# Kernel optimization log

Hardware: AMD Instinct MI355X
Metric: run time of the kernel (lower is better)

Reference implementation:

```python
import jax, jax.numpy as jnp
import numpy as np

DIM = 512
HEADS = 8
DIM_HEAD = 64
HIDDEN = HEADS * DIM_HEAD  # 512
B, N, M = 4, 2048, 2048


def setup_inputs() -> dict:
    key = jax.random.key(0)
    ks = jax.random.split(key, 7)
    s = 0.02
    return {
        "x": jax.random.normal(ks[0], (B, N, DIM), jnp.float32),
        "context": jax.random.normal(ks[1], (B, M, DIM), jnp.float32),
        "Wq": jax.random.normal(ks[2], (DIM, HIDDEN), jnp.float32) * s,
        "Wk": jax.random.normal(ks[3], (DIM, HIDDEN), jnp.float32) * s,
        "Wv": jax.random.normal(ks[4], (DIM, HIDDEN), jnp.float32) * s,
        "Wo": jax.random.normal(ks[5], (HIDDEN, DIM), jnp.float32) * s,
        "bo": jnp.zeros((DIM,), jnp.float32),
    }


def reference(x, context, Wq, Wk, Wv, Wo, bo):
    scale = DIM_HEAD ** (-0.5)
    # projections: [B, N, HIDDEN] -> [B, H, N, D]
    def split_heads(t):
        b, n, _ = t.shape
        return t.reshape(b, n, HEADS, DIM_HEAD).transpose(0, 2, 1, 3)
    q = split_heads(x @ Wq)
    k = split_heads(context @ Wk)
    v = split_heads(context @ Wv)
    # scores: [B, H, N, M]
    sim = jnp.einsum('bhid,bhjd->bhij', q, k) * scale
    attn = jax.nn.softmax(sim, axis=-1)
    out = jnp.einsum('bhij,bhjd->bhid', attn, v)  # [B, H, N, D]
    out = out.transpose(0, 2, 1, 3).reshape(x.shape[0], x.shape[1], HIDDEN)
    return out @ Wo + bo
```

## Files before the change

### kernel.cpp

```cpp
#include <hip/hip_runtime.h>
#include <hip/hip_bf16.h>


typedef __attribute__((ext_vector_type(8))) short bf16x8;
typedef __attribute__((ext_vector_type(4))) float f32x4;

#define MFMA16(a, b, c) __builtin_amdgcn_mfma_f32_16x16x32_bf16(a, b, c, 0, 0, 0)
#define SCALE_LOG2E 0.18033688011112042f

static __device__ inline unsigned short f2b(float f) {
    __hip_bfloat16 h = __float2bfloat16(f);
    return __builtin_bit_cast(unsigned short, h);
}
static __device__ inline unsigned int pk_rnd(float hi, float lo) {
    unsigned uh = __builtin_bit_cast(unsigned, hi) + 0x8000u;
    unsigned ul = __builtin_bit_cast(unsigned, lo) + 0x8000u;
    return __builtin_amdgcn_perm(uh, ul, 0x07060302);
}
static __device__ inline float fexp2(float x) {
    float r;
    asm("v_exp_f32 %0, %1" : "=v"(r) : "v"(x));
    return r;
}
static __device__ inline void gll16(const void* g, void* l) {
    __builtin_amdgcn_global_load_lds(
        (const __attribute__((address_space(1))) void*)g,
        (__attribute__((address_space(3))) void*)l, 16, 0, 0);
}

__global__ __launch_bounds__(256) void prep_kernel(const float* __restrict__ x,
                                                   const float* __restrict__ ctx,
                                                   const float* __restrict__ Wq,
                                                   const float* __restrict__ Wk,
                                                   const float* __restrict__ Wv,
                                                   const float* __restrict__ Wo,
                                                   unsigned short* __restrict__ xb,
                                                   unsigned short* __restrict__ cb,
                                                   unsigned short* __restrict__ wt_base) {
    __shared__ float T[64][65];
    const int bid = blockIdx.x, tid = threadIdx.x;
    if (bid < 8192) {
        const float* src = (bid < 4096) ? x : ctx;
        unsigned short* dst = (bid < 4096) ? xb : cb;
        int i = (bid & 4095) * 256 + tid;
        const float4 v = reinterpret_cast<const float4*>(src)[i];
        uint2 o;
        o.x = pk_rnd(v.y, v.x);
        o.y = pk_rnd(v.w, v.z);
        reinterpret_cast<uint2*>(dst)[i] = o;
        return;
    }
    const int b = bid - 8192;
    const int which = b >> 6, t6 = b & 63;
    const float* W = (which == 0) ? Wq : (which == 1) ? Wk : (which == 2) ? Wv : Wo;
    unsigned short* Wt = wt_base + (size_t)which * 512 * 512;
    const int n0 = (t6 & 7) * 64, k0 = (t6 >> 3) * 64;
    const int rr = tid >> 4, cc = (tid & 15) * 4;
    #pragma unroll
    for (int i = 0; i < 4; i++) {
        const float4 v = *reinterpret_cast<const float4*>(&W[(size_t)(k0 + rr + 16 * i) * 512 + n0 + cc]);
        T[rr + 16 * i][cc + 0] = v.x; T[rr + 16 * i][cc + 1] = v.y;
        T[rr + 16 * i][cc + 2] = v.z; T[rr + 16 * i][cc + 3] = v.w;
    }
    __syncthreads();
    #pragma unroll
    for (int i = 0; i < 4; i++) {
        int n = rr + 16 * i;
        uint2 o;
        o.x = pk_rnd(T[cc + 1][n], T[cc + 0][n]);
        o.y = pk_rnd(T[cc + 3][n], T[cc + 2][n]);
        *reinterpret_cast<uint2*>(&Wt[(size_t)(n0 + n) * 512 + k0 + cc]) = o;
    }
}

__device__ inline void gemm_tile_128(const unsigned short* __restrict__ A,
                                     const unsigned short* __restrict__ Bt,
                                     int row0, int col0, f32x4 acc[4][4]) {
    __shared__ unsigned short As[128 * 32];
    __shared__ unsigned short Bs[128 * 32];
    const int tid  = threadIdx.x;
    const int lane = tid & 63, wave = tid >> 6;
    const int quad = lane >> 4, mr = lane & 15;
    const int m_off = (wave & 1) * 64, n_off = (wave >> 1) * 64;

    const int lrow = lane >> 2;
    const int lq   = (lane & 3) ^ (lrow & 3);
    const unsigned short* aSrc = A  + (size_t)(row0 + wave * 32 + lrow) * 512 + lq * 8;
    const unsigned short* bSrc = Bt + (size_t)(col0 + wave * 32 + lrow) * 512 + lq * 8;
    unsigned short* aL0 = &As[(wave * 32) * 32];
    unsigned short* aL1 = &As[(wave * 32 + 16) * 32];
    unsigned short* bL0 = &Bs[(wave * 32) * 32];
    unsigned short* bL1 = &Bs[(wave * 32 + 16) * 32];

    for (int kt = 0; kt < 16; kt++) {
        __syncthreads();
        gll16(aSrc + kt * 32, aL0);
        gll16(aSrc + 16 * 512 + kt * 32, aL1);
        gll16(bSrc + kt * 32, bL0);
        gll16(bSrc + 16 * 512 + kt * 32, bL1);
        __syncthreads();
        bf16x8 af[4], bfr[4];
        #pragma unroll
        for (int i = 0; i < 4; i++) {
            int m = m_off + i * 16 + mr;
            af[i] = *reinterpret_cast<const bf16x8*>(&As[m * 32 + ((quad ^ (m & 3)) * 8)]);
        }
        #pragma unroll
        for (int j = 0; j < 4; j++) {
            int n = n_off + j * 16 + mr;
            bfr[j] = *reinterpret_cast<const bf16x8*>(&Bs[n * 32 + ((quad ^ (n & 3)) * 8)]);
        }
        #pragma unroll
        for (int i = 0; i < 4; i++)
            #pragma unroll
            for (int j = 0; j < 4; j++)
                acc[i][j] = MFMA16(af[i], bfr[j], acc[i][j]);
    }
}

__global__ __launch_bounds__(256) void gemm_proj_kernel(const unsigned short* __restrict__ xb,
                                                        const unsigned short* __restrict__ cb,
                                                        const unsigned short* __restrict__ wt_base,
                                                        unsigned short* __restrict__ qkv_base) {
    const int f = blockIdx.x, g = f & 7, j = f >> 3;
    const int xt = j & 3;
    const int ry = g + 8 * ((j >> 2) & 7);
    const int which = j >> 5;

    const unsigned short* A  = (which == 0) ? xb : cb;
    const unsigned short* Bt = wt_base + (size_t)which * 512 * 512;
    unsigned short* out      = qkv_base + (size_t)which * 8192 * 512;

    f32x4 acc[4][4];
    #pragma unroll
    for (int i = 0; i < 4; i++)
        #pragma unroll
        for (int j2 = 0; j2 < 4; j2++) acc[i][j2] = (f32x4){0.f, 0.f, 0.f, 0.f};

    gemm_tile_128(A, Bt, ry * 128, xt * 128, acc);

    const int lane = threadIdx.x & 63, wave = threadIdx.x >> 6;
    const int quad = lane >> 4, mr = lane & 15;
    const int m_off = (wave & 1) * 64, n_off = (wave >> 1) * 64;
    const float qs = (which == 0) ? SCALE_LOG2E : 1.0f;

    if (which == 2) {
        #pragma unroll
        for (int i = 0; i < 4; i++) {
            #pragma unroll
            for (int j2 = 0; j2 < 4; j2++) {
                int gcol = xt * 128 + n_off + j2 * 16 + mr;
                int h = gcol >> 6, d = gcol & 63;
                int grow = ry * 128 + m_off + i * 16 + quad * 4;
                int b = grow >> 11, n = grow & 2047;
                int np = (n & ~31) | (((n >> 2) & 3) << 3) | (((n >> 4) & 1) << 2);
                uint2 o;
                o.x = pk_rnd(acc[i][j2][1], acc[i][j2][0]);
                o.y = pk_rnd(acc[i][j2][3], acc[i][j2][2]);
                *reinterpret_cast<uint2*>(&out[((size_t)(b * 8 + h) * 64 + d) * 2048 + np]) = o;
            }
        }
    } else {
        #pragma unroll
        for (int i = 0; i < 4; i++) {
            #pragma unroll
            for (int j2 = 0; j2 < 4; j2++) {
                int gcol = xt * 128 + n_off + j2 * 16 + mr;
                int h = gcol >> 6, d = gcol & 63;
                #pragma unroll
                for (int r = 0; r < 4; r++) {
                    int grow = ry * 128 + m_off + i * 16 + quad * 4 + r;
                    int b = grow >> 11, n = grow & 2047;
                    out[((size_t)(b * 8 + h) * 2048 + n) * 64 + d] = f2b(acc[i][j2][r] * qs);
                }
            }
        }
    }
}

__global__ __launch_bounds__(256) void flash_kernel(const unsigned short* __restrict__ qw,
                                                    const unsigned short* __restrict__ kw,
                                                    const unsigned short* __restrict__ vt,
                                                    unsigned short* __restrict__ ob) {
    __shared__ unsigned short Ks[2][64 * 72];
    __shared__ unsigned short Vs[2][64 * 72];

    const int f = blockIdx.x, g = f & 7, j = f >> 3;
    const int qtile = j & 15;
    const int bh    = g + 8 * (j >> 4);

    const int tid  = threadIdx.x;
    const int lane = tid & 63, wave = tid >> 6;
    const int quad = lane >> 4, mr = lane & 15;

    const unsigned short* qbase = qw + ((size_t)bh * 2048 + qtile * 128 + wave * 32) * 64;
    const unsigned short* kbase = kw + (size_t)bh * 2048 * 64;
    const unsigned short* vbase = vt + (size_t)bh * 64 * 2048;

    bf16x8 qf[2][2];
    #pragma unroll
    for (int gq = 0; gq < 2; gq++) {
        qf[gq][0] = *reinterpret_cast<const bf16x8*>(qbase + (gq * 16 + mr) * 64 + quad * 8);
        qf[gq][1] = *reinterpret_cast<const bf16x8*>(qbase + (gq * 16 + mr) * 64 + 32 + quad * 8);
    }

    bf16x8 ones;
    #pragma unroll
    for (int e = 0; e < 8; e++) ones[e] = (short)0x3F80;

    f32x4 oacc[2][4], lacc[2];
    #pragma unroll
    for (int gq = 0; gq < 2; gq++) {
        lacc[gq] = (f32x4){0.f, 0.f, 0.f, 0.f};
        #pragma unroll
        for (int nt = 0; nt < 4; nt++) oacc[gq][nt] = (f32x4){0.f, 0.f, 0.f, 0.f};
    }

    const int srow = tid >> 2, soff = (tid & 3) * 16;
    const unsigned short* ksrc = kbase + (size_t)srow * 64 + soff;
    const unsigned short* vsrc = vbase + (size_t)srow * 2048 + soff;

    uint4 ka, kb2, va, vb2;
    {
        const uint4* kp = reinterpret_cast<const uint4*>(ksrc);
        ka = kp[0]; kb2 = kp[1];
        const uint4* vp = reinterpret_cast<const uint4*>(vsrc);
        va = vp[0]; vb2 = vp[1];
    }

    #pragma unroll 2
    for (int t = 0; t < 32; ++t) {
        const int cur = t & 1;
        {
            uint4* kd = reinterpret_cast<uint4*>(&Ks[cur][srow * 72 + soff]);
            kd[0] = ka; kd[1] = kb2;
            uint4* vd = reinterpret_cast<uint4*>(&Vs[cur][srow * 72 + soff]);
            vd[0] = va; vd[1] = vb2;
        }
        __syncthreads();
        if (t < 31) {
            const uint4* kp = reinterpret_cast<const uint4*>(ksrc + (size_t)(t + 1) * 64 * 64);
            ka = kp[0]; kb2 = kp[1];
            const uint4* vp = reinterpret_cast<const uint4*>(vsrc + (t + 1) * 64);
            va = vp[0]; vb2 = vp[1];
        }

        f32x4 sv[2][4];
        #pragma unroll
        for (int gq = 0; gq < 2; gq++)
            #pragma unroll
            for (int kt = 0; kt < 4; kt++) sv[gq][kt] = (f32x4){0.f, 0.f, 0.f, 0.f};
        #pragma unroll
        for (int c = 0; c < 2; c++) {
            #pragma unroll
            for (int kt = 0; kt < 4; kt++) {
                bf16x8 kf = *reinterpret_cast<const bf16x8*>(&Ks[cur][(kt * 16 + mr) * 72 + c * 32 + quad * 8]);
                sv[0][kt] = MFMA16(kf, qf[0][c], sv[0][kt]);
                sv[1][kt] = MFMA16(kf, qf[1][c], sv[1][kt]);
            }
        }

        bf16x8 pa[2][2];
        #pragma unroll
        for (int gq = 0; gq < 2; gq++) {
            #pragma unroll
            for (int ks = 0; ks < 2; ks++) {
                uint4 w;
                w.x = pk_rnd(fexp2(sv[gq][2 * ks][1]),     fexp2(sv[gq][2 * ks][0]));
                w.y = pk_rnd(fexp2(sv[gq][2 * ks][3]),     fexp2(sv[gq][2 * ks][2]));
                w.z = pk_rnd(fexp2(sv[gq][2 * ks + 1][1]), fexp2(sv[gq][2 * ks + 1][0]));
                w.w = pk_rnd(fexp2(sv[gq][2 * ks + 1][3]), fexp2(sv[gq][2 * ks + 1][2]));
                pa[gq][ks] = __builtin_bit_cast(bf16x8, w);
            }
        }

        #pragma unroll
        for (int ks = 0; ks < 2; ks++) {
            lacc[0] = MFMA16(pa[0][ks], ones, lacc[0]);
            lacc[1] = MFMA16(pa[1][ks], ones, lacc[1]);
            #pragma unroll
            for (int nt = 0; nt < 4; nt++) {
                bf16x8 vf = *reinterpret_cast<const bf16x8*>(&Vs[cur][(nt * 16 + mr) * 72 + ks * 32 + quad * 8]);
                oacc[0][nt] = MFMA16(pa[0][ks], vf, oacc[0][nt]);
                oacc[1][nt] = MFMA16(pa[1][ks], vf, oacc[1][nt]);
            }
        }
    }

    const int b = bh >> 3, h = bh & 7;
    #pragma unroll
    for (int gq = 0; gq < 2; gq++) {
        #pragma unroll
        for (int r = 0; r < 4; r++) {
            const float li = 1.0f / lacc[gq][r];
            const int row = qtile * 128 + wave * 32 + gq * 16 + quad * 4 + r;
            unsigned short* orow = &ob[((size_t)b * 2048 + row) * 512 + h * 64 + mr];
            #pragma unroll
            for (int nt = 0; nt < 4; nt++)
                orow[nt * 16] = f2b(oacc[gq][nt][r] * li);
        }
    }
}

__global__ __launch_bounds__(256) void gemm_out_kernel(const unsigned short* __restrict__ obuf,
                                                       const unsigned short* __restrict__ Wot,
                                                       const float* __restrict__ bo,
                                                       float* __restrict__ out) {
    const int f = blockIdx.x, g = f & 7, j = f >> 3;
    const int xt = j & 3;
    const int ry = g + 8 * (j >> 2);

    f32x4 acc[4][4];
    #pragma unroll
    for (int i = 0; i < 4; i++)
        #pragma unroll
        for (int j2 = 0; j2 < 4; j2++) acc[i][j2] = (f32x4){0.f, 0.f, 0.f, 0.f};

    gemm_tile_128(obuf, Wot, ry * 128, xt * 128, acc);

    const int lane = threadIdx.x & 63, wave = threadIdx.x >> 6;
    const int quad = lane >> 4, mr = lane & 15;
    const int m_off = (wave & 1) * 64, n_off = (wave >> 1) * 64;
    #pragma unroll
    for (int i = 0; i < 4; i++) {
        #pragma unroll
        for (int j2 = 0; j2 < 4; j2++) {
            int gcol = xt * 128 + n_off + j2 * 16 + mr;
            float bias = bo[gcol];
            #pragma unroll
            for (int r = 0; r < 4; r++) {
                int grow = ry * 128 + m_off + i * 16 + quad * 4 + r;
                out[(size_t)grow * 512 + gcol] = acc[i][j2][r] + bias;
            }
        }
    }
}

extern "C" void kernel_launch(void* const* d_in, const int* in_sizes, int n_in,
                              void* d_out, int out_size, void* d_ws, size_t ws_size,
                              hipStream_t stream) {
    const float* x   = (const float*)d_in[0];
    const float* ctx = (const float*)d_in[1];
    const float* Wq  = (const float*)d_in[2];
    const float* Wk  = (const float*)d_in[3];
    const float* Wv  = (const float*)d_in[4];
    const float* Wo  = (const float*)d_in[5];
    const float* bo  = (const float*)d_in[6];
    float* out = (float*)d_out;

    unsigned short* ws  = (unsigned short*)d_ws;
    unsigned short* xb  = ws;
    unsigned short* cb  = xb + (size_t)8192 * 512;
    unsigned short* Wt  = cb + (size_t)8192 * 512;
    unsigned short* qkv = Wt + (size_t)4 * 512 * 512;
    unsigned short* ob  = qkv + (size_t)3 * 8192 * 512;

    prep_kernel<<<8448, 256, 0, stream>>>(x, ctx, Wq, Wk, Wv, Wo, xb, cb, Wt);
    gemm_proj_kernel<<<768, 256, 0, stream>>>(xb, cb, Wt, qkv);
    flash_kernel<<<512, 256, 0, stream>>>(qkv, qkv + (size_t)8192 * 512,
                                          qkv + (size_t)2 * 8192 * 512, ob);
    gemm_out_kernel<<<256, 256, 0, stream>>>(ob, Wt + (size_t)3 * 512 * 512, bo, out);
}
```

Measured before the change: 173.3 us.

## Load K/V tiles with direct global-to-LDS copies and XOR-swizzled layout

Replaces the register-staged K/V prefetch (global load into registers, then LDS store) in the flash attention loop with gll16 direct global-to-LDS loads into the next buffer. The padded 72-stride LDS rows become unpadded 64-stride rows with an XOR swizzle to avoid bank conflicts. This frees registers and removes the LDS store instructions. The catch is that correctness now depends on the async load's wait/sync being handled inside gll16 or by the single __syncthreads per iteration.

```diff
diff --git a/kernel.cpp b/kernel.cpp
--- a/kernel.cpp
+++ b/kernel.cpp
@@ -182,8 +182,8 @@
                                                     const unsigned short* __restrict__ kw,
                                                     const unsigned short* __restrict__ vt,
                                                     unsigned short* __restrict__ ob) {
-    __shared__ unsigned short Ks[2][64 * 72];
-    __shared__ unsigned short Vs[2][64 * 72];
+    __shared__ unsigned short Ks[2][64 * 64];
+    __shared__ unsigned short Vs[2][64 * 64];
 
     const int f = blockIdx.x, g = f & 7, j = f >> 3;
     const int qtile = j & 15;
@@ -216,33 +216,33 @@
         for (int nt = 0; nt < 4; nt++) oacc[gq][nt] = (f32x4){0.f, 0.f, 0.f, 0.f};
     }
 
-    const int srow = tid >> 2, soff = (tid & 3) * 16;
-    const unsigned short* ksrc = kbase + (size_t)srow * 64 + soff;
-    const unsigned short* vsrc = vbase + (size_t)srow * 2048 + soff;
-
-    uint4 ka, kb2, va, vb2;
-    {
-        const uint4* kp = reinterpret_cast<const uint4*>(ksrc);
-        ka = kp[0]; kb2 = kp[1];
-        const uint4* vp = reinterpret_cast<const uint4*>(vsrc);
-        va = vp[0]; vb2 = vp[1];
-    }
+    const int lrow8 = lane >> 3;
+    const int lswz  = ((lane & 7) ^ lrow8) * 8;
+    const int krow0 = wave * 16 + lrow8;
+    const int koff0 = krow0 * 64 + lswz;
+    const int koff1 = (krow0 + 8) * 64 + lswz;
+    const size_t voff0 = (size_t)krow0 * 2048 + lswz;
+    const size_t voff1 = (size_t)(krow0 + 8) * 2048 + lswz;
+    unsigned short* kd0[2] = {&Ks[0][(wave * 16) * 64], &Ks[1][(wave * 16) * 64]};
+    unsigned short* vd0[2] = {&Vs[0][(wave * 16) * 64], &Vs[1][(wave * 16) * 64]};
+
+    gll16(kbase + koff0, kd0[0]);
+    gll16(kbase + koff1, kd0[0] + 8 * 64);
+    gll16(vbase + voff0, vd0[0]);
+    gll16(vbase + voff1, vd0[0] + 8 * 64);
 
     #pragma unroll 2
     for (int t = 0; t < 32; ++t) {
         const int cur = t & 1;
-        {
-            uint4* kd = reinterpret_cast<uint4*>(&Ks[cur][srow * 72 + soff]);
-            kd[0] = ka; kd[1] = kb2;
-            uint4* vd = reinterpret_cast<uint4*>(&Vs[cur][srow * 72 + soff]);
-            vd[0] = va; vd[1] = vb2;
-        }
         __syncthreads();
         if (t < 31) {
-            const uint4* kp = reinterpret_cast<const uint4*>(ksrc + (size_t)(t + 1) * 64 * 64);
-            ka = kp[0]; kb2 = kp[1];
-            const uint4* vp = reinterpret_cast<const uint4*>(vsrc + (t + 1) * 64);
-            va = vp[0]; vb2 = vp[1];
+            const int nxt = cur ^ 1;
+            const size_t kt_ = (size_t)(t + 1) * 4096;
+            const int vt_ = (t + 1) * 64;
+            gll16(kbase + kt_ + koff0, kd0[nxt]);
+            gll16(kbase + kt_ + koff1, kd0[nxt] + 8 * 64);
+            gll16(vbase + vt_ + voff0, vd0[nxt]);
+            gll16(vbase + vt_ + voff1, vd0[nxt] + 8 * 64);
         }
 
         f32x4 sv[2][4];
@@ -254,7 +254,8 @@
         for (int c = 0; c < 2; c++) {
             #pragma unroll
             for (int kt = 0; kt < 4; kt++) {
-                bf16x8 kf = *reinterpret_cast<const bf16x8*>(&Ks[cur][(kt * 16 + mr) * 72 + c * 32 + quad * 8]);
+                bf16x8 kf = *reinterpret_cast<const bf16x8*>(
+                    &Ks[cur][(kt * 16 + mr) * 64 + (((c * 4 + quad) ^ (mr & 7)) * 8)]);
                 sv[0][kt] = MFMA16(kf, qf[0][c], sv[0][kt]);
                 sv[1][kt] = MFMA16(kf, qf[1][c], sv[1][kt]);
             }
@@ -280,7 +281,8 @@
             lacc[1] = MFMA16(pa[1][ks], ones, lacc[1]);
             #pragma unroll
             for (int nt = 0; nt < 4; nt++) {
-                bf16x8 vf = *reinterpret_cast<const bf16x8*>(&Vs[cur][(nt * 16 + mr) * 72 + ks * 32 + quad * 8]);
+                bf16x8 vf = *reinterpret_cast<const bf16x8*>(
+                    &Vs[cur][(nt * 16 + mr) * 64 + (((ks * 4 + quad) ^ (mr & 7)) * 8)]);
                 oacc[0][nt] = MFMA16(pa[0][ks], vf, oacc[0][nt]);
                 oacc[1][nt] = MFMA16(pa[1][ks], vf, oacc[1][nt]);
             }
```

Result: no change. 171.6 us (-1.0%).
